# Kernel optimization log

Measured on AMD Instinct MI355X. Metric: run time of the kernel, lower is better.

Reference implementation:

```python
import jax, jax.numpy as jnp
import numpy as np

B, L, S, D = 32, 256, 4, 512
H = L * S  # history_capacity
TGB = 128
VOCAB = 50000
LN_EPS = 1e-5


def _layer_norm(x, gamma, beta):
    mu = jnp.mean(x, axis=-1, keepdims=True)
    var = jnp.var(x, axis=-1, keepdims=True)
    return (x - mu) * jax.lax.rsqrt(var + LN_EPS) * gamma + beta


def setup_inputs() -> dict:
    key = jax.random.key(0)
    ks = jax.random.split(key, 16)
    inp = {
        'embed_table': jax.random.normal(ks[0], (VOCAB, D), jnp.float32) * 0.02,
        'time_gap_emb': jax.random.normal(ks[1], (TGB + 1, D), jnp.float32) * 0.02,
        'seq_id_emb': jax.random.normal(ks[2], (S + 1, D), jnp.float32) * 0.02,
        'pos_emb': jax.random.normal(ks[3], (L, D), jnp.float32) * 0.02,
        'ln_gamma': jnp.ones((5 * D,), jnp.float32),
        'ln_beta': jnp.zeros((5 * D,), jnp.float32),
        'w1': jax.random.normal(ks[4], (5 * D, 4 * D), jnp.float32) * (1.0 / np.sqrt(5 * D)),
        'b1': jnp.zeros((4 * D,), jnp.float32),
        'w2': jax.random.normal(ks[5], (4 * D, D), jnp.float32) * (1.0 / np.sqrt(4 * D)),
        'b2': jnp.zeros((D,), jnp.float32),
        'empty_tokens': jax.random.normal(ks[6], (S, D), jnp.float32) * 0.02,
        'history_tokens': jax.random.randint(ks[7], (B, H), 0, VOCAB, jnp.int64 if jax.config.jax_enable_x64 else jnp.int32),
        'post_tokens': jax.random.randint(ks[8], (B, H), 0, VOCAB),
        'author_tokens': jax.random.randint(ks[9], (B, H), 0, VOCAB),
        'action_tokens': jax.random.randint(ks[10], (B, H), 0, VOCAB),
        'time_gap': jax.random.randint(ks[11], (B, H), 0, TGB + 1),
        'group_ids': jax.random.randint(ks[12], (B, H), 0, S + 1),
        'lengths': jax.random.randint(ks[13], (B,), 0, H + 1),
    }
    return inp


def reference(embed_table, time_gap_emb, seq_id_emb, pos_emb, ln_gamma, ln_beta,
              w1, b1, w2, b2, empty_tokens,
              history_tokens, post_tokens, author_tokens, action_tokens,
              time_gap, group_ids, lengths):
    # padded-dense validity mask: positions < lengths  [B,H]
    history_mask = jnp.arange(H)[None, :] < lengths[:, None]
    # zero out padded tokens (to_padded_dense pads with 0)
    hm_i = history_mask.astype(history_tokens.dtype)
    ht = history_tokens * hm_i
    pt = post_tokens * hm_i
    at = author_tokens * hm_i
    ct = action_tokens * hm_i
    tg = jnp.clip(time_gap * hm_i, 0, TGB)
    gid = group_ids * hm_i

    # event feature: 4 token embeds + time-gap embed -> [B,H,5D]
    event_inputs = jnp.concatenate(
        [embed_table[ht], embed_table[pt], embed_table[at], embed_table[ct],
         time_gap_emb[tg]], axis=-1)
    x = _layer_norm(event_inputs, ln_gamma, ln_beta)
    h = jax.nn.silu(x @ w1 + b1)          # dropout is eval-mode no-op
    event_tokens = h @ w2 + b2            # [B,H,D]

    # per-(batch, group) bucketization: keep last L valid positions of each group
    grp = jnp.arange(1, S + 1)
    mask_bs = history_mask[:, None, :] & (gid[:, None, :] == grp[None, :, None])  # [B,S,H]
    cum = jnp.cumsum(mask_bs.astype(jnp.int32), axis=-1)
    count = cum[..., -1]                                  # [B,S]
    offset = jnp.maximum(count - L, 0)                    # drop all but last L
    rank0 = cum - 1
    keep = mask_bs & (rank0 >= offset[..., None])
    dest = jnp.where(keep, rank0 - offset[..., None], L)  # slot L = dump slot

    def scatter_one(tokens, d):  # tokens [H,D], d [H] -> [L,D]
        return jnp.zeros((L + 1, D), tokens.dtype).at[d].set(tokens)[:L]

    # vmap over batch then group
    states = jax.vmap(lambda tok, ds: jax.vmap(lambda d: scatter_one(tok, d))(ds))(
        event_tokens, dest)                               # [B,S,L,D]

    # empty groups get the learned empty token at slot 0
    is_empty = (count == 0)                               # [B,S]
    slot0 = (jnp.arange(L) == 0)                          # [L]
    states = jnp.where((is_empty[:, :, None] & slot0[None, None, :])[..., None],
                       empty_tokens[None, :, None, :], states)
    kept = jnp.where(is_empty, 1, jnp.minimum(count, L))  # [B,S]
    sequence_mask = jnp.arange(L)[None, None, :] < kept[..., None]  # [B,S,L]

    states = states + pos_emb[None, None, :, :] + seq_id_emb[1:][None, :, None, :]
    states = states * sequence_mask[..., None].astype(states.dtype)
    return states, sequence_mask
```

## Files before the change

### kernel.cpp

```cpp
#include <hip/hip_runtime.h>
#include <hip/hip_bf16.h>
#include <stdint.h>

#define NB 32
#define NL 256
#define NS 4
#define ND 512
#define NH 1024
#define FIVE_D 2560
#define HID 2048
#define MMAX 32768
#define CHUNK 8192
#define NCHUNK 4

typedef __bf16 bf16_t;
typedef __bf16 bf16x8 __attribute__((ext_vector_type(8)));
typedef float f32x4 __attribute__((ext_vector_type(4)));

__device__ __forceinline__ void async_ld16(const void* g, void* l) {
  __builtin_amdgcn_global_load_lds(
      (__attribute__((address_space(1))) void*)(uintptr_t)g,
      (__attribute__((address_space(3))) void*)(uintptr_t)l, 16, 0, 0);
}

__global__ void build_index_kernel(const int* __restrict__ group_ids,
                                   const int* __restrict__ lengths,
                                   int* __restrict__ n_rows,
                                   int* __restrict__ kept_eff,
                                   int* __restrict__ row_src,
                                   int* __restrict__ row_dst) {
  const int g = blockIdx.x;
  const int b = g >> 2, s = g & 3;
  const int t = threadIdx.x;
  const int lane = t & 63, w = t >> 6;
  int len = lengths[b];
  len = len < 0 ? 0 : (len > NH ? NH : len);
  const int* gi = group_ids + b * NH;

  __shared__ int wtot[16];
  __shared__ int sbase;

  bool valid[4];
#pragma unroll
  for (int c = 0; c < 4; ++c) {
    int h = c * 256 + t;
    valid[c] = (h < len) && (gi[h] == s + 1);
    unsigned long long m = __ballot(valid[c]);
    if (lane == 0) wtot[c * 4 + w] = __popcll(m);
  }
  __syncthreads();

  int pre[16];
  int run = 0;
#pragma unroll
  for (int i = 0; i < 16; ++i) { pre[i] = run; run += wtot[i]; }
  const int count = run;
  const int keff = count < NL ? count : NL;
  const int offset = count - keff;

  if (t == 0) {
    kept_eff[g] = keff;
    sbase = atomicAdd(n_rows, keff);
  }
  __syncthreads();
  const int base = sbase;

  const unsigned long long lt = (1ull << lane) - 1ull;
#pragma unroll
  for (int c = 0; c < 4; ++c) {
    unsigned long long m = __ballot(valid[c]);
    if (valid[c]) {
      int rank = pre[c * 4 + w] + __popcll(m & lt);
      if (rank >= offset) {
        int slot = rank - offset;
        row_src[base + slot] = b * NH + c * 256 + t;
        row_dst[base + slot] = g * NL + slot;
      }
    }
  }
}

template <int KD, int NDIM>
__global__ void transpose_cvt_kernel(const float* __restrict__ src,
                                     bf16_t* __restrict__ dst) {
  __shared__ float tile[32][33];
  int k0 = blockIdx.y * 32, n0 = blockIdx.x * 32;
  int tx = threadIdx.x & 31, ty = threadIdx.x >> 5;
#pragma unroll
  for (int i = 0; i < 32; i += 8)
    tile[ty + i][tx] = src[(size_t)(k0 + ty + i) * NDIM + n0 + tx];
  __syncthreads();
#pragma unroll
  for (int i = 0; i < 32; i += 8)
    dst[(size_t)(n0 + ty + i) * KD + k0 + tx] = (bf16_t)tile[tx][ty + i];
}

__global__ void gather_ln_kernel(const float* __restrict__ embed,
                                 const float* __restrict__ tg_emb,
                                 const int* __restrict__ ht,
                                 const int* __restrict__ pt,
                                 const int* __restrict__ at,
                                 const int* __restrict__ ct,
                                 const int* __restrict__ tg,
                                 const float* __restrict__ gamma,
                                 const float* __restrict__ beta,
                                 const int* __restrict__ n_rows,
                                 const int* __restrict__ row_src,
                                 int row_base,
                                 bf16_t* __restrict__ X) {
  int rl = blockIdx.x;
  int r = row_base + rl;
  if (r >= *n_rows) return;
  int pos = row_src[r];
  int t = threadIdx.x;

  const float* seg[5];
  seg[0] = embed + (size_t)ht[pos] * ND;
  seg[1] = embed + (size_t)pt[pos] * ND;
  seg[2] = embed + (size_t)at[pos] * ND;
  seg[3] = embed + (size_t)ct[pos] * ND;
  int tgv = tg[pos];
  tgv = tgv < 0 ? 0 : (tgv > 128 ? 128 : tgv);
  seg[4] = tg_emb + (size_t)tgv * ND;

  float v[10];
  float sum = 0.f, sq = 0.f;
#pragma unroll
  for (int i = 0; i < 10; ++i) {
    int c = t + i * 256;
    v[i] = seg[c >> 9][c & 511];
    sum += v[i];
    sq += v[i] * v[i];
  }
#pragma unroll
  for (int off = 32; off > 0; off >>= 1) {
    sum += __shfl_down(sum, off);
    sq += __shfl_down(sq, off);
  }
  __shared__ float red[8];
  int wv = t >> 6, ln = t & 63;
  if (ln == 0) { red[wv] = sum; red[4 + wv] = sq; }
  __syncthreads();
  float S = red[0] + red[1] + red[2] + red[3];
  float Q = red[4] + red[5] + red[6] + red[7];
  float mu = S * (1.f / FIVE_D);
  float var = Q * (1.f / FIVE_D) - mu * mu;
  float rstd = rsqrtf(var + 1e-5f);

  bf16_t* xr = X + (size_t)rl * FIVE_D;
#pragma unroll
  for (int i = 0; i < 10; ++i) {
    int c = t + i * 256;
    xr[c] = (bf16_t)((v[i] - mu) * rstd * gamma[c] + beta[c]);
  }
}

#define FENCE asm volatile("" ::: "memory")
#define BARRIER do { FENCE; __builtin_amdgcn_s_barrier(); FENCE; } while (0)
#define WAIT_VM(n) asm volatile("s_waitcnt vmcnt(" #n ")" ::: "memory")

template <int KD, int LDC>
__launch_bounds__(512, 2)
__global__ void gemm256_kernel(const bf16_t* __restrict__ A,
                               const bf16_t* __restrict__ Bt,
                               const int* __restrict__ nrows_p,
                               int row_base,
                               const float* __restrict__ bias,
                               bf16_t* __restrict__ Cb) {
  static_assert(KD % 64 == 0 && KD / 64 >= 2, "KD");
  const int M = *nrows_p;
  const int m0 = blockIdx.y * 256;
  if (row_base + m0 >= M) return;
  const int n0 = blockIdx.x * 256;

  extern __shared__ char smem[];

  const int t = threadIdx.x;
  const int lane = t & 63;
  const int wv = t >> 6;
  const int wm = wv >> 2;
  const int wn = wv & 3;
  const int l15 = lane & 15;
  const int l4 = lane >> 4;

  const int r0 = t >> 3;
  const int sq = (t & 7) ^ (r0 & 7);
  const bf16_t* Ab = A + (size_t)(m0 + r0) * KD + sq * 8;
  const bf16_t* Bb = Bt + (size_t)(n0 + r0) * KD + sq * 8;
  const int dst16 = t * 16;

  const int cs0 = (l4 ^ (l15 & 7)) << 4;
  const int cs1 = cs0 ^ 64;
  const int arow = (wm * 128 + l15) * 128;
  const int brow = (wn * 64 + l15) * 128;

  f32x4 acc[2][2][4][2] = {};
  bf16x8 a[4][2], bl[2][2], bh[2][2];

#define STAGE_A(dbuf, h, kofs)                                               \
  do {                                                                       \
    char* _d = smem + (dbuf) * 65536 + (h) * 16384 + dst16;                  \
    async_ld16(Ab + (size_t)((h) * 128) * KD + (kofs), _d);                  \
    async_ld16(Ab + (size_t)((h) * 128 + 64) * KD + (kofs), _d + 8192);      \
  } while (0)
#define STAGE_B(dbuf, h, kofs)                                               \
  do {                                                                       \
    char* _d = smem + (dbuf) * 65536 + 32768 + (h) * 16384 + dst16;          \
    async_ld16(Bb + (size_t)((h) * 128) * KD + (kofs), _d);                  \
    async_ld16(Bb + (size_t)((h) * 128 + 64) * KD + (kofs), _d + 8192);      \
  } while (0)
#define LOAD_A(cbuf, mh)                                                     \
  do {                                                                       \
    const char* _s = smem + (cbuf) * 65536 + (mh) * 8192 + arow;             \
    _Pragma("unroll") for (int _i = 0; _i < 4; ++_i) {                       \
      a[_i][0] = *(const bf16x8*)(_s + _i * 2048 + cs0);                     \
      a[_i][1] = *(const bf16x8*)(_s + _i * 2048 + cs1);                     \
    }                                                                        \
  } while (0)
#define LOAD_B(dst, cbuf, nh)                                                \
  do {                                                                       \
    const char* _s = smem + (cbuf) * 65536 + 32768 + (nh) * 4096 + brow;     \
    _Pragma("unroll") for (int _j = 0; _j < 2; ++_j) {                       \
      dst[_j][0] = *(const bf16x8*)(_s + _j * 2048 + cs0);                   \
      dst[_j][1] = *(const bf16x8*)(_s + _j * 2048 + cs1);                   \
    }                                                                        \
  } while (0)
#define MMA(mh, nh, B)                                                       \
  do {                                                                       \
    _Pragma("unroll") for (int _i = 0; _i < 4; ++_i)                         \
    _Pragma("unroll") for (int _j = 0; _j < 2; ++_j) {                       \
      acc[mh][nh][_i][_j] = __builtin_amdgcn_mfma_f32_16x16x32_bf16(         \
          a[_i][0], B[_j][0], acc[mh][nh][_i][_j], 0, 0, 0);                 \
      acc[mh][nh][_i][_j] = __builtin_amdgcn_mfma_f32_16x16x32_bf16(         \
          a[_i][1], B[_j][1], acc[mh][nh][_i][_j], 0, 0, 0);                 \
    }                                                                        \
  } while (0)

  constexpr int NT = KD / 64;

  STAGE_A(0, 0, 0);
  STAGE_A(0, 1, 0);
  STAGE_B(0, 0, 0);
  STAGE_B(0, 1, 0);

  int c = 0;
  for (int tk = 1; tk < NT; ++tk) {
    const int kn = tk * 64;
    const int d = c ^ 1;
    STAGE_A(d, 0, kn);
    STAGE_A(d, 1, kn);
    WAIT_VM(4);
    BARRIER;
    LOAD_A(c, 0);
    LOAD_B(bl, c, 0);
    __builtin_amdgcn_s_setprio(1);
    MMA(0, 0, bl);
    __builtin_amdgcn_s_setprio(0);
    STAGE_B(d, 0, kn);
    STAGE_B(d, 1, kn);
    LOAD_B(bh, c, 1);
    __builtin_amdgcn_s_setprio(1);
    MMA(0, 1, bh);
    __builtin_amdgcn_s_setprio(0);
    LOAD_A(c, 1);
    __builtin_amdgcn_s_setprio(1);
    MMA(1, 1, bh);
    MMA(1, 0, bl);
    __builtin_amdgcn_s_setprio(0);
    BARRIER;
    c = d;
  }

  WAIT_VM(0);
  BARRIER;
  LOAD_A(c, 0);
  LOAD_B(bl, c, 0);
  MMA(0, 0, bl);
  LOAD_B(bh, c, 1);
  MMA(0, 1, bh);
  LOAD_A(c, 1);
  MMA(1, 1, bh);
  MMA(1, 0, bl);

#pragma unroll
  for (int mh = 0; mh < 2; ++mh)
#pragma unroll
    for (int i = 0; i < 4; ++i) {
      const int rbase = m0 + wm * 128 + mh * 64 + i * 16 + l4 * 4;
#pragma unroll
      for (int nh = 0; nh < 2; ++nh)
#pragma unroll
        for (int j = 0; j < 2; ++j) {
          const int n = n0 + wn * 64 + nh * 32 + j * 16 + l15;
          const float bn = bias[n];
#pragma unroll
          for (int q = 0; q < 4; ++q) {
            float v = acc[mh][nh][i][j][q] + bn;
            v = v / (1.f + __expf(-v));
            Cb[(size_t)(rbase + q) * LDC + n] = (bf16_t)v;
          }
        }
    }
#undef STAGE_A
#undef STAGE_B
#undef LOAD_A
#undef LOAD_B
#undef MMA
}

template <int KD>
__launch_bounds__(512, 2)
__global__ void gemm128_scatter_kernel(const bf16_t* __restrict__ A,
                                       const bf16_t* __restrict__ Bt,
                                       const int* __restrict__ nrows_p,
                                       int row_base,
                                       const float* __restrict__ bias,
                                       const int* __restrict__ row_dst,
                                       const float* __restrict__ pos_emb,
                                       const float* __restrict__ seq_emb,
                                       float* __restrict__ out) {
  static_assert(KD % 64 == 0 && KD / 64 >= 2, "KD");
  const int M = *nrows_p;
  const int m0 = blockIdx.y * 128;
  if (row_base + m0 >= M) return;
  const int n0 = blockIdx.x * 128;

  extern __shared__ char smem[];

  const int t = threadIdx.x;
  const int lane = t & 63;
  const int wv = t >> 6;
  const int wm = wv >> 1;
  const int wn = wv & 1;
  const int l15 = lane & 15;
  const int l4 = lane >> 4;

  const int r0 = t >> 3;
  const int sq = (t & 7) ^ (r0 & 7);
  const bf16_t* Ab = A + (size_t)(m0 + r0) * KD + sq * 8;
  const bf16_t* Bb = Bt + (size_t)(n0 + r0) * KD + sq * 8;
  const int dst16 = t * 16;

  const int cs0 = (l4 ^ (l15 & 7)) << 4;
  const int cs1 = cs0 ^ 64;
  const int arow = (wm * 32 + l15) * 128;
  const int brow = (wn * 64 + l15) * 128;

  f32x4 acc[2][4] = {};
  bf16x8 a[2][2], b[4][2];

#define STAGE_A2(dbuf, kofs)                                                 \
  do {                                                                       \
    char* _d = smem + (dbuf) * 32768 + dst16;                                \
    async_ld16(Ab + (kofs), _d);                                             \
    async_ld16(Ab + (size_t)64 * KD + (kofs), _d + 8192);                    \
  } while (0)
#define STAGE_B2(dbuf, kofs)                                                 \
  do {                                                                       \
    char* _d = smem + (dbuf) * 32768 + 16384 + dst16;                        \
    async_ld16(Bb + (kofs), _d);                                             \
    async_ld16(Bb + (size_t)64 * KD + (kofs), _d + 8192);                    \
  } while (0)
#define LOAD_A2(cbuf)                                                        \
  do {                                                                       \
    const char* _s = smem + (cbuf) * 32768 + arow;                           \
    _Pragma("unroll") for (int _i = 0; _i < 2; ++_i) {                       \
      a[_i][0] = *(const bf16x8*)(_s + _i * 2048 + cs0);                     \
      a[_i][1] = *(const bf16x8*)(_s + _i * 2048 + cs1);                     \
    }                                                                        \
  } while (0)
#define LOAD_B2(cbuf)                                                        \
  do {                                                                       \
    const char* _s = smem + (cbuf) * 32768 + 16384 + brow;                   \
    _Pragma("unroll") for (int _j = 0; _j < 4; ++_j) {                       \
      b[_j][0] = *(const bf16x8*)(_s + _j * 2048 + cs0);                     \
      b[_j][1] = *(const bf16x8*)(_s + _j * 2048 + cs1);                     \
    }                                                                        \
  } while (0)
#define MMA2                                                                 \
  do {                                                                       \
    _Pragma("unroll") for (int _i = 0; _i < 2; ++_i)                         \
    _Pragma("unroll") for (int _j = 0; _j < 4; ++_j) {                       \
      acc[_i][_j] = __builtin_amdgcn_mfma_f32_16x16x32_bf16(                 \
          a[_i][0], b[_j][0], acc[_i][_j], 0, 0, 0);                         \
      acc[_i][_j] = __builtin_amdgcn_mfma_f32_16x16x32_bf16(                 \
          a[_i][1], b[_j][1], acc[_i][_j], 0, 0, 0);                         \
    }                                                                        \
  } while (0)

  constexpr int NT = KD / 64;

  STAGE_A2(0, 0);
  STAGE_B2(0, 0);

  int c = 0;
  for (int tk = 1; tk < NT; ++tk) {
    const int kn = tk * 64;
    const int d = c ^ 1;
    STAGE_A2(d, kn);
    WAIT_VM(2);
    BARRIER;
    LOAD_A2(c);
    LOAD_B2(c);
    STAGE_B2(d, kn);
    __builtin_amdgcn_s_setprio(1);
    MMA2;
    __builtin_amdgcn_s_setprio(0);
    BARRIER;
    c = d;
  }

  WAIT_VM(0);
  BARRIER;
  LOAD_A2(c);
  LOAD_B2(c);
  MMA2;

#pragma unroll
  for (int i = 0; i < 2; ++i) {
    int mbase = m0 + wm * 32 + i * 16 + l4 * 4;
#pragma unroll
    for (int q = 0; q < 4; ++q) {
      int r = mbase + q;
      if (row_base + r >= M) continue;
      int dst = row_dst[row_base + r];
      int slot = dst & (NL - 1);
      int sg = (dst >> 8) & 3;
#pragma unroll
      for (int j = 0; j < 4; ++j) {
        int n = n0 + wn * 64 + j * 16 + l15;
        float v = acc[i][j][q] + bias[n] + pos_emb[slot * ND + n] +
                  seq_emb[(sg + 1) * ND + n];
        out[(size_t)dst * ND + n] = v;
      }
    }
  }
#undef STAGE_A2
#undef STAGE_B2
#undef LOAD_A2
#undef LOAD_B2
#undef MMA2
}

__global__ void fill_bg_kernel(const int* __restrict__ kept_eff,
                               const float* __restrict__ empty_tokens,
                               const float* __restrict__ pos_emb,
                               const float* __restrict__ seq_emb,
                               float* __restrict__ out,
                               float* __restrict__ mask) {
  int g = blockIdx.x;
  int s = g & 3;
  int t = threadIdx.x;
  int ce = kept_eff[g];
  bool empty = (ce == 0);
  int keptm = empty ? 1 : ce;

  mask[g * NL + t] = (t < keptm) ? 1.f : 0.f;

  float* base = out + (size_t)g * NL * ND;
  if (empty) {
    for (int d = t; d < ND; d += 256)
      base[d] = empty_tokens[s * ND + d] + pos_emb[d] + seq_emb[(s + 1) * ND + d];
  }
  int start = empty ? 1 : ce;
  uint4* p = (uint4*)base;
  uint4 z; z.x = z.y = z.z = z.w = 0u;
  for (int i = start * (ND / 4) + t; i < NL * (ND / 4); i += 256) p[i] = z;
}

extern "C" void kernel_launch(void* const* d_in, const int* in_sizes, int n_in,
                              void* d_out, int out_size, void* d_ws,
                              size_t ws_size, hipStream_t stream) {
  const float* embed_table = (const float*)d_in[0];
  const float* time_gap_emb = (const float*)d_in[1];
  const float* seq_id_emb = (const float*)d_in[2];
  const float* pos_emb = (const float*)d_in[3];
  const float* ln_gamma = (const float*)d_in[4];
  const float* ln_beta = (const float*)d_in[5];
  const float* w1 = (const float*)d_in[6];
  const float* b1 = (const float*)d_in[7];
  const float* w2 = (const float*)d_in[8];
  const float* b2 = (const float*)d_in[9];
  const float* empty_tokens = (const float*)d_in[10];
  const int* history_tokens = (const int*)d_in[11];
  const int* post_tokens = (const int*)d_in[12];
  const int* author_tokens = (const int*)d_in[13];
  const int* action_tokens = (const int*)d_in[14];
  const int* time_gap = (const int*)d_in[15];
  const int* group_ids = (const int*)d_in[16];
  const int* lengths = (const int*)d_in[17];

  char* ws = (char*)d_ws;
  int* n_rows = (int*)ws;
  int* kept_eff = (int*)(ws + 256);
  int* row_src = (int*)(ws + 4096);
  int* row_dst = (int*)(ws + 4096 + 131072);
  bf16_t* W1T = (bf16_t*)(ws + 266240);
  bf16_t* W2T = W1T + (size_t)HID * FIVE_D;
  bf16_t* Xc = W2T + (size_t)ND * HID;
  bf16_t* H1c = Xc + (size_t)CHUNK * FIVE_D;

  float* out_states = (float*)d_out;
  float* out_mask = out_states + (size_t)NB * NS * NL * ND;

  (void)hipFuncSetAttribute(
      reinterpret_cast<const void*>(gemm256_kernel<FIVE_D, HID>),
      hipFuncAttributeMaxDynamicSharedMemorySize, 131072);
  (void)hipFuncSetAttribute(
      reinterpret_cast<const void*>(gemm128_scatter_kernel<HID>),
      hipFuncAttributeMaxDynamicSharedMemorySize, 65536);

  hipMemsetAsync(n_rows, 0, 4, stream);

  build_index_kernel<<<NB * NS, 256, 0, stream>>>(group_ids, lengths, n_rows,
                                                  kept_eff, row_src, row_dst);

  transpose_cvt_kernel<FIVE_D, HID>
      <<<dim3(HID / 32, FIVE_D / 32), 256, 0, stream>>>(w1, W1T);
  transpose_cvt_kernel<HID, ND>
      <<<dim3(ND / 32, HID / 32), 256, 0, stream>>>(w2, W2T);

  for (int c = 0; c < NCHUNK; ++c) {
    int row_base = c * CHUNK;
    gather_ln_kernel<<<CHUNK, 256, 0, stream>>>(
        embed_table, time_gap_emb, history_tokens, post_tokens, author_tokens,
        action_tokens, time_gap, ln_gamma, ln_beta, n_rows, row_src, row_base,
        Xc);

    gemm256_kernel<FIVE_D, HID>
        <<<dim3(HID / 256, CHUNK / 256), 512, 131072, stream>>>(
            Xc, W1T, n_rows, row_base, b1, H1c);

    gemm128_scatter_kernel<HID>
        <<<dim3(ND / 128, CHUNK / 128), 512, 65536, stream>>>(
            H1c, W2T, n_rows, row_base, b2, row_dst, pos_emb, seq_id_emb,
            out_states);
  }

  fill_bg_kernel<<<NB * NS, 256, 0, stream>>>(kept_eff, empty_tokens, pos_emb,
                                              seq_id_emb, out_states, out_mask);
}
```

Before: 449.3 us.

## Fuse background fill into index build, vectorize gather-LN, size chunks from workspace

The background zero-fill and mask writes now run inside build_index_kernel, which removes the separate fill_bg launch. The gather+layernorm kernel becomes grid-strided with a fixed 2048 blocks and uses float4 loads and bf16x4 stores. The chunk size is chosen at runtime from the workspace size, up to a single 32768-row chunk, which cuts the number of launches and GEMM tail waves. One risk is ordering: the zero-fill now happens before the scatter GEMM writes rows, which is fine because the filled and scattered regions do not overlap.

```diff
diff --git a/kernel.cpp b/kernel.cpp
--- a/kernel.cpp
+++ b/kernel.cpp
@@ -10,10 +10,9 @@
 #define FIVE_D 2560
 #define HID 2048
 #define MMAX 32768
-#define CHUNK 8192
-#define NCHUNK 4
 
 typedef __bf16 bf16_t;
+typedef __bf16 bf16x4 __attribute__((ext_vector_type(4)));
 typedef __bf16 bf16x8 __attribute__((ext_vector_type(8)));
 typedef float f32x4 __attribute__((ext_vector_type(4)));
 
@@ -26,9 +25,13 @@
 __global__ void build_index_kernel(const int* __restrict__ group_ids,
                                    const int* __restrict__ lengths,
                                    int* __restrict__ n_rows,
-                                   int* __restrict__ kept_eff,
                                    int* __restrict__ row_src,
-                                   int* __restrict__ row_dst) {
+                                   int* __restrict__ row_dst,
+                                   const float* __restrict__ empty_tokens,
+                                   const float* __restrict__ pos_emb,
+                                   const float* __restrict__ seq_emb,
+                                   float* __restrict__ out,
+                                   float* __restrict__ mask) {
   const int g = blockIdx.x;
   const int b = g >> 2, s = g & 3;
   const int t = threadIdx.x;
@@ -58,10 +61,7 @@
   const int keff = count < NL ? count : NL;
   const int offset = count - keff;
 
-  if (t == 0) {
-    kept_eff[g] = keff;
-    sbase = atomicAdd(n_rows, keff);
-  }
+  if (t == 0) sbase = atomicAdd(n_rows, keff);
   __syncthreads();
   const int base = sbase;
 
@@ -78,6 +78,21 @@
       }
     }
   }
+
+  const bool empty = (count == 0);
+  const int keptm = empty ? 1 : keff;
+  mask[g * NL + t] = (t < keptm) ? 1.f : 0.f;
+
+  float* basep = out + (size_t)g * NL * ND;
+  if (empty) {
+    for (int d = t; d < ND; d += 256)
+      basep[d] = empty_tokens[s * ND + d] + pos_emb[d] +
+                 seq_emb[(s + 1) * ND + d];
+  }
+  int start = empty ? 1 : keff;
+  uint4* p = (uint4*)basep;
+  uint4 z; z.x = z.y = z.z = z.w = 0u;
+  for (int i = start * (ND / 4) + t; i < NL * (ND / 4); i += 256) p[i] = z;
 }
 
 template <int KD, int NDIM>
@@ -106,52 +121,92 @@
                                  const float* __restrict__ beta,
                                  const int* __restrict__ n_rows,
                                  const int* __restrict__ row_src,
-                                 int row_base,
+                                 int row_base, int chunk,
                                  bf16_t* __restrict__ X) {
-  int rl = blockIdx.x;
-  int r = row_base + rl;
-  if (r >= *n_rows) return;
-  int pos = row_src[r];
-  int t = threadIdx.x;
-
-  const float* seg[5];
-  seg[0] = embed + (size_t)ht[pos] * ND;
-  seg[1] = embed + (size_t)pt[pos] * ND;
-  seg[2] = embed + (size_t)at[pos] * ND;
-  seg[3] = embed + (size_t)ct[pos] * ND;
-  int tgv = tg[pos];
-  tgv = tgv < 0 ? 0 : (tgv > 128 ? 128 : tgv);
-  seg[4] = tg_emb + (size_t)tgv * ND;
-
-  float v[10];
-  float sum = 0.f, sq = 0.f;
-#pragma unroll
-  for (int i = 0; i < 10; ++i) {
-    int c = t + i * 256;
-    v[i] = seg[c >> 9][c & 511];
-    sum += v[i];
-    sq += v[i] * v[i];
-  }
-#pragma unroll
-  for (int off = 32; off > 0; off >>= 1) {
-    sum += __shfl_down(sum, off);
-    sq += __shfl_down(sq, off);
-  }
+  const int t = threadIdx.x;
+  const int M = *n_rows;
+  int lim = row_base + chunk;
+  if (lim > M) lim = M;
+
   __shared__ float red[8];
-  int wv = t >> 6, ln = t & 63;
-  if (ln == 0) { red[wv] = sum; red[4 + wv] = sq; }
-  __syncthreads();
-  float S = red[0] + red[1] + red[2] + red[3];
-  float Q = red[4] + red[5] + red[6] + red[7];
-  float mu = S * (1.f / FIVE_D);
-  float var = Q * (1.f / FIVE_D) - mu * mu;
-  float rstd = rsqrtf(var + 1e-5f);
-
-  bf16_t* xr = X + (size_t)rl * FIVE_D;
-#pragma unroll
-  for (int i = 0; i < 10; ++i) {
-    int c = t + i * 256;
-    xr[c] = (bf16_t)((v[i] - mu) * rstd * gamma[c] + beta[c]);
+
+  const int i0 = t;
+  const int i1 = 256 + t;
+  const int i2 = 512 + t;
+  const int s0 = i0 >> 7, o0 = (i0 & 127) * 4;
+  const int s1 = i1 >> 7, o1 = (i1 & 127) * 4;
+  const int o2 = (i2 & 127) * 4;
+  const bool has2 = (t < 128);
+
+  for (int r = row_base + blockIdx.x; r < lim; r += gridDim.x) {
+    const int rl = r - row_base;
+    const int pos = row_src[r];
+
+    const float* seg[5];
+    seg[0] = embed + (size_t)ht[pos] * ND;
+    seg[1] = embed + (size_t)pt[pos] * ND;
+    seg[2] = embed + (size_t)at[pos] * ND;
+    seg[3] = embed + (size_t)ct[pos] * ND;
+    int tgv = tg[pos];
+    tgv = tgv < 0 ? 0 : (tgv > 128 ? 128 : tgv);
+    seg[4] = tg_emb + (size_t)tgv * ND;
+
+    float4 v0 = *(const float4*)(seg[s0] + o0);
+    float4 v1 = *(const float4*)(seg[s1] + o1);
+    float4 v2 = make_float4(0.f, 0.f, 0.f, 0.f);
+    if (has2) v2 = *(const float4*)(seg[4] + o2);
+
+    float sum = v0.x + v0.y + v0.z + v0.w + v1.x + v1.y + v1.z + v1.w +
+                v2.x + v2.y + v2.z + v2.w;
+    float sq = v0.x * v0.x + v0.y * v0.y + v0.z * v0.z + v0.w * v0.w +
+               v1.x * v1.x + v1.y * v1.y + v1.z * v1.z + v1.w * v1.w +
+               v2.x * v2.x + v2.y * v2.y + v2.z * v2.z + v2.w * v2.w;
+#pragma unroll
+    for (int off = 32; off > 0; off >>= 1) {
+      sum += __shfl_down(sum, off);
+      sq += __shfl_down(sq, off);
+    }
+    int wv = t >> 6, ln = t & 63;
+    if (ln == 0) { red[wv] = sum; red[4 + wv] = sq; }
+    __syncthreads();
+    float S = red[0] + red[1] + red[2] + red[3];
+    float Q = red[4] + red[5] + red[6] + red[7];
+    float mu = S * (1.f / FIVE_D);
+    float var = Q * (1.f / FIVE_D) - mu * mu;
+    float rstd = rsqrtf(var + 1e-5f);
+
+    bf16_t* xr = X + (size_t)rl * FIVE_D;
+    {
+      float4 gm = *(const float4*)(gamma + i0 * 4);
+      float4 bt = *(const float4*)(beta + i0 * 4);
+      bf16x4 wv4;
+      wv4[0] = (bf16_t)((v0.x - mu) * rstd * gm.x + bt.x);
+      wv4[1] = (bf16_t)((v0.y - mu) * rstd * gm.y + bt.y);
+      wv4[2] = (bf16_t)((v0.z - mu) * rstd * gm.z + bt.z);
+      wv4[3] = (bf16_t)((v0.w - mu) * rstd * gm.w + bt.w);
+      *(bf16x4*)(xr + i0 * 4) = wv4;
+    }
+    {
+      float4 gm = *(const float4*)(gamma + i1 * 4);
+      float4 bt = *(const float4*)(beta + i1 * 4);
+      bf16x4 wv4;
+      wv4[0] = (bf16_t)((v1.x - mu) * rstd * gm.x + bt.x);
+      wv4[1] = (bf16_t)((v1.y - mu) * rstd * gm.y + bt.y);
+      wv4[2] = (bf16_t)((v1.z - mu) * rstd * gm.z + bt.z);
+      wv4[3] = (bf16_t)((v1.w - mu) * rstd * gm.w + bt.w);
+      *(bf16x4*)(xr + i1 * 4) = wv4;
+    }
+    if (has2) {
+      float4 gm = *(const float4*)(gamma + i2 * 4);
+      float4 bt = *(const float4*)(beta + i2 * 4);
+      bf16x4 wv4;
+      wv4[0] = (bf16_t)((v2.x - mu) * rstd * gm.x + bt.x);
+      wv4[1] = (bf16_t)((v2.y - mu) * rstd * gm.y + bt.y);
+      wv4[2] = (bf16_t)((v2.z - mu) * rstd * gm.z + bt.z);
+      wv4[3] = (bf16_t)((v2.w - mu) * rstd * gm.w + bt.w);
+      *(bf16x4*)(xr + i2 * 4) = wv4;
+    }
+    __syncthreads();
   }
 }
 
@@ -442,32 +497,6 @@
 #undef MMA2
 }
 
-__global__ void fill_bg_kernel(const int* __restrict__ kept_eff,
-                               const float* __restrict__ empty_tokens,
-                               const float* __restrict__ pos_emb,
-                               const float* __restrict__ seq_emb,
-                               float* __restrict__ out,
-                               float* __restrict__ mask) {
-  int g = blockIdx.x;
-  int s = g & 3;
-  int t = threadIdx.x;
-  int ce = kept_eff[g];
-  bool empty = (ce == 0);
-  int keptm = empty ? 1 : ce;
-
-  mask[g * NL + t] = (t < keptm) ? 1.f : 0.f;
-
-  float* base = out + (size_t)g * NL * ND;
-  if (empty) {
-    for (int d = t; d < ND; d += 256)
-      base[d] = empty_tokens[s * ND + d] + pos_emb[d] + seq_emb[(s + 1) * ND + d];
-  }
-  int start = empty ? 1 : ce;
-  uint4* p = (uint4*)base;
-  uint4 z; z.x = z.y = z.z = z.w = 0u;
-  for (int i = start * (ND / 4) + t; i < NL * (ND / 4); i += 256) p[i] = z;
-}
-
 extern "C" void kernel_launch(void* const* d_in, const int* in_sizes, int n_in,
                               void* d_out, int out_size, void* d_ws,
                               size_t ws_size, hipStream_t stream) {
@@ -490,15 +519,20 @@
   const int* group_ids = (const int*)d_in[16];
   const int* lengths = (const int*)d_in[17];
 
+  const size_t fixed = 266240 + (size_t)(HID * FIVE_D + ND * HID) * 2;
+  int chunk, nchunk;
+  if (ws_size >= fixed + (size_t)32768 * 9216) { chunk = 32768; nchunk = 1; }
+  else if (ws_size >= fixed + (size_t)16384 * 9216) { chunk = 16384; nchunk = 2; }
+  else { chunk = 8192; nchunk = 4; }
+
   char* ws = (char*)d_ws;
   int* n_rows = (int*)ws;
-  int* kept_eff = (int*)(ws + 256);
   int* row_src = (int*)(ws + 4096);
   int* row_dst = (int*)(ws + 4096 + 131072);
   bf16_t* W1T = (bf16_t*)(ws + 266240);
   bf16_t* W2T = W1T + (size_t)HID * FIVE_D;
   bf16_t* Xc = W2T + (size_t)ND * HID;
-  bf16_t* H1c = Xc + (size_t)CHUNK * FIVE_D;
+  bf16_t* H1c = Xc + (size_t)chunk * FIVE_D;
 
   float* out_states = (float*)d_out;
   float* out_mask = out_states + (size_t)NB * NS * NL * ND;
@@ -512,31 +546,29 @@
 
   hipMemsetAsync(n_rows, 0, 4, stream);
 
-  build_index_kernel<<<NB * NS, 256, 0, stream>>>(group_ids, lengths, n_rows,
-                                                  kept_eff, row_src, row_dst);
+  build_index_kernel<<<NB * NS, 256, 0, stream>>>(
+      group_ids, lengths, n_rows, row_src, row_dst, empty_tokens, pos_emb,
+      seq_id_emb, out_states, out_mask);
 
   transpose_cvt_kernel<FIVE_D, HID>
       <<<dim3(HID / 32, FIVE_D / 32), 256, 0, stream>>>(w1, W1T);
   transpose_cvt_kernel<HID, ND>
       <<<dim3(ND / 32, HID / 32), 256, 0, stream>>>(w2, W2T);
 
-  for (int c = 0; c < NCHUNK; ++c) {
-    int row_base = c * CHUNK;
-    gather_ln_kernel<<<CHUNK, 256, 0, stream>>>(
+  for (int c = 0; c < nchunk; ++c) {
+    int row_base = c * chunk;
+    gather_ln_kernel<<<2048, 256, 0, stream>>>(
         embed_table, time_gap_emb, history_tokens, post_tokens, author_tokens,
         action_tokens, time_gap, ln_gamma, ln_beta, n_rows, row_src, row_base,
-        Xc);
+        chunk, Xc);
 
     gemm256_kernel<FIVE_D, HID>
-        <<<dim3(HID / 256, CHUNK / 256), 512, 131072, stream>>>(
+        <<<dim3(HID / 256, chunk / 256), 512, 131072, stream>>>(
             Xc, W1T, n_rows, row_base, b1, H1c);
 
     gemm128_scatter_kernel<HID>
-        <<<dim3(ND / 128, CHUNK / 128), 512, 65536, stream>>>(
+        <<<dim3(ND / 128, chunk / 128), 512, 65536, stream>>>(
             H1c, W2T, n_rows, row_base, b2, row_dst, pos_emb, seq_id_emb,
             out_states);
   }
-
-  fill_bg_kernel<<<NB * NS, 256, 0, stream>>>(kept_eff, empty_tokens, pos_emb,
-                                              seq_id_emb, out_states, out_mask);
-}
+}
```

After: 414.3 us. -7.8%, faster.
